# Kernel tuning notes

Measured on AMD Instinct MI355X. Metric: run time of the kernel, lower is better.

## Reference

```python
import math
import jax, jax.numpy as jnp
import numpy as np

HEADS = 16
MODEL = 1024
KEY = 64
VAL = 64
B, S = 4, 2048


def setup_inputs() -> dict:
    key = jax.random.key(0)
    ks = jax.random.split(key, 8)
    queries = jax.random.normal(ks[0], (B, S, MODEL), dtype=jnp.float32)
    keys_ = jax.random.normal(ks[1], (B, S, MODEL), dtype=jnp.float32)
    values = jax.random.normal(ks[2], (B, S, MODEL), dtype=jnp.float32)
    # causal boolean mask, true = attention allowed (every row has >=1 True)
    masks = jnp.broadcast_to(jnp.tril(jnp.ones((S, S), dtype=bool)), (B, S, S))
    lim_in = 1.0 / math.sqrt(MODEL)
    # stacked per-head projection weights, stored as [H, model, head_dim]
    Wq = jax.random.uniform(ks[3], (HEADS, MODEL, KEY), minval=-lim_in, maxval=lim_in, dtype=jnp.float32)
    Wk = jax.random.uniform(ks[4], (HEADS, MODEL, KEY), minval=-lim_in, maxval=lim_in, dtype=jnp.float32)
    Wv = jax.random.uniform(ks[5], (HEADS, MODEL, VAL), minval=-lim_in, maxval=lim_in, dtype=jnp.float32)
    lim_o = 1.0 / math.sqrt(HEADS * VAL)
    Wo = jax.random.uniform(ks[6], (HEADS * VAL, MODEL), minval=-lim_o, maxval=lim_o, dtype=jnp.float32)
    bo = jax.random.uniform(ks[7], (MODEL,), minval=-lim_o, maxval=lim_o, dtype=jnp.float32)
    return {"queries": queries, "keys": keys_, "values": values, "masks": masks,
            "Wq": Wq, "Wk": Wk, "Wv": Wv, "Wo": Wo, "bo": bo}


def reference(queries, keys, values, masks, Wq, Wk, Wv, Wo, bo):
    # per-head projections, batched over heads: [B,S,M] x [H,M,D] -> [B,H,S,D]
    q = jnp.einsum('bsm,hmd->bhsd', queries, Wq)
    k = jnp.einsum('bsm,hmd->bhsd', keys, Wk)
    v = jnp.einsum('bsm,hmd->bhsd', values, Wv)
    scale = 1.0 / math.sqrt(KEY)
    scores = jnp.einsum('bhqd,bhkd->bhqk', q, k) * scale  # [B,H,Q,K]
    scores = jnp.where(masks[:, None, :, :], scores, -jnp.inf)
    weights = jax.nn.softmax(scores, axis=-1)
    out = jnp.einsum('bhqk,bhkv->bhqv', weights, v)  # [B,H,Q,V]
    # concat heads along feature dim (head-major order matches torch concat)
    out = out.transpose(0, 2, 1, 3).reshape(B, S, HEADS * VAL)
    return out @ Wo + bo
```

## Files before the change

### kernel.cpp

```cpp
#include <hip/hip_runtime.h>


typedef __bf16 bf16;
typedef __attribute__((ext_vector_type(8))) __bf16 bf16x8;
typedef __attribute__((ext_vector_type(4))) __bf16 bf16x4;
typedef __attribute__((ext_vector_type(4))) float f32x4;
typedef unsigned int u32;

#define GLB_AS __attribute__((address_space(1)))
#define LDS_AS __attribute__((address_space(3)))

#define L2E 1.44269504088896340736f

static __device__ __forceinline__ void stage_swz(const bf16* __restrict__ g, long ldelem,
                                                 long row0, long col0,
                                                 bf16* lds, int rows, int tid)
{
    const int lane = tid & 63;
    const int wave = tid >> 6;
    const int nch = rows >> 3;
    for (int c = wave; c < nch; c += 4) {
        unsigned o  = ((unsigned)c << 10) + ((unsigned)lane << 4);
        unsigned r  = o >> 7;
        unsigned cb = o & 127u;
        unsigned cs = cb ^ ((r & 7u) << 4);
        const bf16* src = g + (row0 + (long)r) * ldelem + col0 + (long)(cs >> 1);
        char* dst = (char*)lds + ((unsigned)c << 10);
        __builtin_amdgcn_global_load_lds((GLB_AS u32*)src, (LDS_AS u32*)dst, 16, 0, 0);
    }
}

__global__ void cast3(const float4* __restrict__ a, const float4* __restrict__ b,
                      const float4* __restrict__ c,
                      bf16x4* __restrict__ xa, bf16x4* __restrict__ xb,
                      bf16x4* __restrict__ xc)
{
    const int n4 = (8192 * 1024) / 4;
    for (int i = blockIdx.x * blockDim.x + threadIdx.x; i < n4; i += gridDim.x * blockDim.x) {
        float4 v;
        v = a[i]; xa[i] = (bf16x4){(bf16)v.x, (bf16)v.y, (bf16)v.z, (bf16)v.w};
        v = b[i]; xb[i] = (bf16x4){(bf16)v.x, (bf16)v.y, (bf16)v.z, (bf16)v.w};
        v = c[i]; xc[i] = (bf16x4){(bf16)v.x, (bf16)v.y, (bf16)v.z, (bf16)v.w};
    }
}

__global__ void transw(const float* __restrict__ wq, const float* __restrict__ wk,
                       const float* __restrict__ wv, const float* __restrict__ wo,
                       bf16* __restrict__ wqT, bf16* __restrict__ wkT,
                       bf16* __restrict__ wvT, bf16* __restrict__ woT)
{
    __shared__ float t[64][65];
    const int tid = threadIdx.x, bx = blockIdx.x, by = blockIdx.y;
    const float* srcs[3] = {wq, wk, wv};
    bf16* dsts[3] = {wqT, wkT, wvT};
#pragma unroll
    for (int m = 0; m < 3; ++m) {
        const float sc = (m == 0) ? 0.125f : 1.0f;
        for (int i = tid; i < 4096; i += 256) {
            int r = i >> 6, c = i & 63;
            t[c][r] = srcs[m][by * 65536 + (bx * 64 + r) * 64 + c];
        }
        __syncthreads();
        for (int i = tid; i < 4096; i += 256) {
            int r = i >> 6, c = i & 63;
            dsts[m][(long)(by * 64 + r) * 1024 + bx * 64 + c] = (bf16)(t[r][c] * sc);
        }
        __syncthreads();
    }
    for (int i = tid; i < 4096; i += 256) {
        int r = i >> 6, c = i & 63;
        t[c][r] = wo[(long)(bx * 64 + r) * 1024 + by * 64 + c];
    }
    __syncthreads();
    for (int i = tid; i < 4096; i += 256) {
        int r = i >> 6, c = i & 63;
        woT[(long)(by * 64 + r) * 1024 + bx * 64 + c] = (bf16)t[r][c];
    }
}

template<int MODE>
static __device__ __forceinline__ void gemm_body(const bf16* __restrict__ A,
                                                 const bf16* __restrict__ Bt,
                                                 bf16* __restrict__ Cb,
                                                 float* __restrict__ Cf,
                                                 const float* __restrict__ bias,
                                                 long row0, long col0,
                                                 bf16* sA, bf16* sB)
{
    const int tid = threadIdx.x, lane = tid & 63, wave = tid >> 6;
    const int wr = wave >> 1, wc = wave & 1;

    f32x4 acc[4][4];
#pragma unroll
    for (int i = 0; i < 4; ++i)
#pragma unroll
        for (int j = 0; j < 4; ++j) acc[i][j] = (f32x4){0.f, 0.f, 0.f, 0.f};

    for (int kt = 0; kt < 16; ++kt) {
        __syncthreads();
        stage_swz(A,  1024, row0, (long)kt << 6, sA, 128, tid);
        stage_swz(Bt, 1024, col0, (long)kt << 6, sB, 128, tid);
        __syncthreads();
#pragma unroll
        for (int kk = 0; kk < 2; ++kk) {
            bf16x8 af[4], bfr[4];
            const unsigned kb = (unsigned)(kk << 6) + (unsigned)((lane >> 4) << 4);
#pragma unroll
            for (int i = 0; i < 4; ++i) {
                unsigned r = (unsigned)((wr << 6) + (i << 4) + (lane & 15));
                af[i] = *(const bf16x8*)((const char*)sA + (r << 7) + (kb ^ ((r & 7u) << 4)));
            }
#pragma unroll
            for (int j = 0; j < 4; ++j) {
                unsigned r = (unsigned)((wc << 6) + (j << 4) + (lane & 15));
                bfr[j] = *(const bf16x8*)((const char*)sB + (r << 7) + (kb ^ ((r & 7u) << 4)));
            }
#pragma unroll
            for (int i = 0; i < 4; ++i)
#pragma unroll
                for (int j = 0; j < 4; ++j)
                    acc[i][j] = __builtin_amdgcn_mfma_f32_16x16x32_bf16(af[i], bfr[j], acc[i][j], 0, 0, 0);
        }
    }

#pragma unroll
    for (int i = 0; i < 4; ++i) {
#pragma unroll
        for (int j = 0; j < 4; ++j) {
#pragma unroll
            for (int rr = 0; rr < 4; ++rr) {
                long row = row0 + (wr << 6) + (i << 4) + ((lane >> 4) << 2) + rr;
                long col = col0 + (wc << 6) + (j << 4) + (lane & 15);
                float v = acc[i][j][rr];
                if constexpr (MODE == 2) {
                    Cf[row * 1024 + col] = v + bias[col];
                } else if constexpr (MODE == 0) {
                    long idx = (((row >> 11) << 4) + (col >> 6)) * 131072 + (row & 2047) * 64 + (col & 63);
                    Cb[idx] = (bf16)v;
                } else {
                    long idx = ((((col >> 11) << 4) + (row >> 6)) * 64 + (row & 63)) * 2048 + (col & 2047);
                    Cb[idx] = (bf16)v;
                }
            }
        }
    }
}

__global__ __launch_bounds__(256, 3) void gemm_qkv(const bf16* __restrict__ Xq, const bf16* __restrict__ WqT, bf16* __restrict__ qp,
                                                   const bf16* __restrict__ Xk, const bf16* __restrict__ WkT, bf16* __restrict__ kp,
                                                   const bf16* __restrict__ WvT, const bf16* __restrict__ Xv, bf16* __restrict__ vTp)
{
    __shared__ alignas(16) bf16 sA[128 * 64];
    __shared__ alignas(16) bf16 sB[128 * 64];
    const int bx = blockIdx.x;
    if (blockIdx.y == 0)
        gemm_body<0>(Xq, WqT, qp, nullptr, nullptr, (long)(bx >> 3) << 7, (long)(bx & 7) << 7, sA, sB);
    else if (blockIdx.y == 1)
        gemm_body<0>(Xk, WkT, kp, nullptr, nullptr, (long)(bx >> 3) << 7, (long)(bx & 7) << 7, sA, sB);
    else
        gemm_body<3>(WvT, Xv, vTp, nullptr, nullptr, (long)(bx & 7) << 7, (long)(bx >> 3) << 7, sA, sB);
}

__global__ __launch_bounds__(256, 3) void gemm_out(const bf16* __restrict__ A, const bf16* __restrict__ Bt,
                                                   float* __restrict__ Cf, const float* __restrict__ bias)
{
    __shared__ alignas(16) bf16 sA[128 * 64];
    __shared__ alignas(16) bf16 sB[128 * 64];
    gemm_body<2>(A, Bt, nullptr, Cf, bias, (long)blockIdx.x << 7, (long)blockIdx.y << 7, sA, sB);
}

__global__ __launch_bounds__(256, 2) void attn(const bf16* __restrict__ q,
                                               const bf16* __restrict__ k,
                                               const bf16* __restrict__ vT,
                                               bf16* __restrict__ o)
{
    __shared__ alignas(16) bf16 sK[2][64 * 64];
    __shared__ alignas(16) bf16 sV[2][64 * 64];
    __shared__ alignas(16) bf16 sP[4][32 * 72];
    const int tid = threadIdx.x, lane = tid & 63, wave = tid >> 6;
    const int bid = blockIdx.x;
    const int hb = ((bid & 7) << 3) + ((bid >> 3) & 7);
    const int pair = bid >> 6;
    const int h = hb & 15, b = hb >> 4;
    const bf16* qh = q  + (long)hb * 131072;
    const bf16* kh = k  + (long)hb * 131072;
    const bf16* vh = vT + (long)hb * 131072;

    bf16x8 vone;
#pragma unroll
    for (int i = 0; i < 8; ++i) vone[i] = (bf16)1.0f;

    for (int half = 0; half < 2; ++half) {
        const int qt = half ? (15 - pair) : pair;
        const int qw = (qt << 7) + (wave << 5);

        bf16x8 aq[2][2];
#pragma unroll
        for (int mf = 0; mf < 2; ++mf)
#pragma unroll
            for (int kk = 0; kk < 2; ++kk)
                aq[mf][kk] = *(const bf16x8*)(qh + (long)(qw + (mf << 4) + (lane & 15)) * 64
                                                 + (kk << 5) + ((lane >> 4) << 3));

        f32x4 accO[2][4], accOl[2];
        float mrow[2][4];
#pragma unroll
        for (int mf = 0; mf < 2; ++mf) {
#pragma unroll
            for (int nf = 0; nf < 4; ++nf) accO[mf][nf] = (f32x4){0.f, 0.f, 0.f, 0.f};
            accOl[mf] = (f32x4){0.f, 0.f, 0.f, 0.f};
#pragma unroll
            for (int rr = 0; rr < 4; ++rr) mrow[mf][rr] = -1e30f;
        }

        const int nkv = (qt << 1) + 2;
        __syncthreads();
        stage_swz(kh, 64,   0, 0, sK[0], 64, tid);
        stage_swz(vh, 2048, 0, 0, sV[0], 64, tid);

        for (int kvt = 0; kvt < nkv; ++kvt) {
            const int cur = kvt & 1;
            const int kv0 = kvt << 6;
            __syncthreads();
            if (kvt + 1 < nkv) {
                stage_swz(kh, 64,   (long)(kv0 + 64), 0, sK[cur ^ 1], 64, tid);
                stage_swz(vh, 2048, 0, (long)(kv0 + 64), sV[cur ^ 1], 64, tid);
            }
            if (kv0 > qw + 31) continue;

            f32x4 s[2][4];
#pragma unroll
            for (int mf = 0; mf < 2; ++mf)
#pragma unroll
                for (int nf = 0; nf < 4; ++nf) s[mf][nf] = (f32x4){0.f, 0.f, 0.f, 0.f};
#pragma unroll
            for (int kk = 0; kk < 2; ++kk) {
                bf16x8 bk[4];
                const unsigned kb = (unsigned)(kk << 6) + (unsigned)((lane >> 4) << 4);
#pragma unroll
                for (int nf = 0; nf < 4; ++nf) {
                    unsigned r = (unsigned)((nf << 4) + (lane & 15));
                    bk[nf] = *(const bf16x8*)((const char*)sK[cur] + (r << 7) + (kb ^ ((r & 7u) << 4)));
                }
#pragma unroll
                for (int mf = 0; mf < 2; ++mf)
#pragma unroll
                    for (int nf = 0; nf < 4; ++nf)
                        s[mf][nf] = __builtin_amdgcn_mfma_f32_16x16x32_bf16(aq[mf][kk], bk[nf], s[mf][nf], 0, 0, 0);
            }

            if (kv0 + 63 > qw) {
#pragma unroll
                for (int mf = 0; mf < 2; ++mf)
#pragma unroll
                    for (int rr = 0; rr < 4; ++rr) {
                        const int ra = qw + (mf << 4) + ((lane >> 4) << 2) + rr;
#pragma unroll
                        for (int nf = 0; nf < 4; ++nf)
                            if ((kv0 + (nf << 4) + (lane & 15)) > ra) s[mf][nf][rr] = -1e30f;
                    }
            }

#pragma unroll
            for (int mf = 0; mf < 2; ++mf) {
#pragma unroll
                for (int rr = 0; rr < 4; ++rr) {
                    float mt = fmaxf(fmaxf(s[mf][0][rr], s[mf][1][rr]), fmaxf(s[mf][2][rr], s[mf][3][rr]));
                    mt = fmaxf(mt, __shfl_xor(mt, 1));
                    mt = fmaxf(mt, __shfl_xor(mt, 2));
                    mt = fmaxf(mt, __shfl_xor(mt, 4));
                    mt = fmaxf(mt, __shfl_xor(mt, 8));
                    if (mt > mrow[mf][rr]) {
                        const float cf = __builtin_exp2f((mrow[mf][rr] - mt) * L2E);
                        mrow[mf][rr] = mt;
                        accOl[mf][rr] *= cf;
#pragma unroll
                        for (int nf = 0; nf < 4; ++nf) accO[mf][nf][rr] *= cf;
                    }
                    const float m2 = mrow[mf][rr] * L2E;
#pragma unroll
                    for (int nf = 0; nf < 4; ++nf)
                        s[mf][nf][rr] = __builtin_exp2f(__builtin_fmaf(s[mf][nf][rr], L2E, -m2));
                }
            }

            bf16* pw = &sP[wave][0];
#pragma unroll
            for (int mf = 0; mf < 2; ++mf)
#pragma unroll
                for (int nf = 0; nf < 4; ++nf)
#pragma unroll
                    for (int rr = 0; rr < 4; ++rr)
                        pw[((mf << 4) + ((lane >> 4) << 2) + rr) * 72 + (nf << 4) + (lane & 15)] =
                            (bf16)s[mf][nf][rr];

#pragma unroll
            for (int kk = 0; kk < 2; ++kk) {
                bf16x8 pa[2], bv[4];
#pragma unroll
                for (int mf = 0; mf < 2; ++mf)
                    pa[mf] = *(const bf16x8*)(pw + ((mf << 4) + (lane & 15)) * 72
                                                 + (kk << 5) + ((lane >> 4) << 3));
                const unsigned kb = (unsigned)(kk << 6) + (unsigned)((lane >> 4) << 4);
#pragma unroll
                for (int nf = 0; nf < 4; ++nf) {
                    unsigned r = (unsigned)((nf << 4) + (lane & 15));
                    bv[nf] = *(const bf16x8*)((const char*)sV[cur] + (r << 7) + (kb ^ ((r & 7u) << 4)));
                }
#pragma unroll
                for (int mf = 0; mf < 2; ++mf) {
#pragma unroll
                    for (int nf = 0; nf < 4; ++nf)
                        accO[mf][nf] = __builtin_amdgcn_mfma_f32_16x16x32_bf16(pa[mf], bv[nf], accO[mf][nf], 0, 0, 0);
                    accOl[mf] = __builtin_amdgcn_mfma_f32_16x16x32_bf16(pa[mf], vone, accOl[mf], 0, 0, 0);
                }
            }
        }

#pragma unroll
        for (int mf = 0; mf < 2; ++mf)
#pragma unroll
            for (int rr = 0; rr < 4; ++rr) {
                const float inv = 1.f / accOl[mf][rr];
                const long ra = qw + (mf << 4) + ((lane >> 4) << 2) + rr;
#pragma unroll
                for (int nf = 0; nf < 4; ++nf)
                    o[((long)b * 2048 + ra) * 1024 + (h << 6) + (nf << 4) + (lane & 15)] =
                        (bf16)(accO[mf][nf][rr] * inv);
            }
    }
}

extern "C" void kernel_launch(void* const* d_in, const int* in_sizes, int n_in,
                              void* d_out, int out_size, void* d_ws, size_t ws_size,
                              hipStream_t stream)
{
    const float* queries = (const float*)d_in[0];
    const float* keys    = (const float*)d_in[1];
    const float* values  = (const float*)d_in[2];
    const float* Wq = (const float*)d_in[4];
    const float* Wk = (const float*)d_in[5];
    const float* Wv = (const float*)d_in[6];
    const float* Wo = (const float*)d_in[7];
    const float* bo = (const float*)d_in[8];
    float* out = (float*)d_out;

    bf16* Xq  = (bf16*)d_ws;
    bf16* Xk  = Xq  + 8388608;
    bf16* Xv  = Xk  + 8388608;
    bf16* WqT = Xv  + 8388608;
    bf16* WkT = WqT + 1048576;
    bf16* WvT = WkT + 1048576;
    bf16* WoT = WvT + 1048576;
    bf16* qp  = WoT + 1048576;
    bf16* kp  = qp  + 8388608;
    bf16* vTp = Xq;
    bf16* ao  = Xk;
    if (ws_size < (size_t)92274688) return;

    cast3<<<dim3(2048), dim3(256), 0, stream>>>((const float4*)queries, (const float4*)keys,
                                                (const float4*)values,
                                                (bf16x4*)Xq, (bf16x4*)Xk, (bf16x4*)Xv);
    transw<<<dim3(16, 16), dim3(256), 0, stream>>>(Wq, Wk, Wv, Wo, WqT, WkT, WvT, WoT);
    gemm_qkv<<<dim3(512, 3), dim3(256), 0, stream>>>(Xq, WqT, qp, Xk, WkT, kp, WvT, Xv, vTp);
    attn<<<dim3(512), dim3(256), 0, stream>>>(qp, kp, vTp, ao);
    gemm_out<<<dim3(64, 8), dim3(256), 0, stream>>>(ao, WoT, out, bo);
}
```

Baseline: 440.3 us.

## Transpose score MFMA so softmax rows reduce in-lane with lazy rescaling

Swaps the MFMA operands so each lane holds one query row's scores across registers. The row max then needs only two cross-lane shuffles instead of four per register row. The running max is updated only when it grows by more than a threshold, and the accumulator rescale is skipped for the whole wave unless some lane updated. P is written to LDS as packed 4-element vector stores. Together these cut shuffle, exp and LDS store instructions in the softmax, at the cost of slightly larger unnormalized exponent values that bf16/fp32 must absorb.

```diff
diff --git a/kernel.cpp b/kernel.cpp
--- a/kernel.cpp
+++ b/kernel.cpp
@@ -203,14 +203,13 @@
                                                  + (kk << 5) + ((lane >> 4) << 3));
 
         f32x4 accO[2][4], accOl[2];
-        float mrow[2][4];
+        float mrow[2];
 #pragma unroll
         for (int mf = 0; mf < 2; ++mf) {
 #pragma unroll
             for (int nf = 0; nf < 4; ++nf) accO[mf][nf] = (f32x4){0.f, 0.f, 0.f, 0.f};
             accOl[mf] = (f32x4){0.f, 0.f, 0.f, 0.f};
-#pragma unroll
-            for (int rr = 0; rr < 4; ++rr) mrow[mf][rr] = -1e30f;
+            mrow[mf] = -1e30f;
         }
 
         const int nkv = (qt << 1) + 2;
@@ -246,60 +245,75 @@
                 for (int mf = 0; mf < 2; ++mf)
 #pragma unroll
                     for (int nf = 0; nf < 4; ++nf)
-                        s[mf][nf] = __builtin_amdgcn_mfma_f32_16x16x32_bf16(aq[mf][kk], bk[nf], s[mf][nf], 0, 0, 0);
-            }
+                        s[mf][nf] = __builtin_amdgcn_mfma_f32_16x16x32_bf16(bk[nf], aq[mf][kk], s[mf][nf], 0, 0, 0);
+            }
+
+            const int g4 = (lane >> 4) << 2;
 
             if (kv0 + 63 > qw) {
 #pragma unroll
+                for (int mf = 0; mf < 2; ++mf) {
+                    const int qv = qw + (mf << 4) + (lane & 15);
+#pragma unroll
+                    for (int nf = 0; nf < 4; ++nf)
+#pragma unroll
+                        for (int reg = 0; reg < 4; ++reg)
+                            if (kv0 + (nf << 4) + g4 + reg > qv) s[mf][nf][reg] = -1e30f;
+                }
+            }
+
+            bool upAny = false;
+            float cfl[2];
+#pragma unroll
+            for (int mf = 0; mf < 2; ++mf) {
+                float m0 = fmaxf(fmaxf(s[mf][0][0], s[mf][0][1]), fmaxf(s[mf][0][2], s[mf][0][3]));
+                float m1 = fmaxf(fmaxf(s[mf][1][0], s[mf][1][1]), fmaxf(s[mf][1][2], s[mf][1][3]));
+                float m2_ = fmaxf(fmaxf(s[mf][2][0], s[mf][2][1]), fmaxf(s[mf][2][2], s[mf][2][3]));
+                float m3 = fmaxf(fmaxf(s[mf][3][0], s[mf][3][1]), fmaxf(s[mf][3][2], s[mf][3][3]));
+                float mt = fmaxf(fmaxf(m0, m1), fmaxf(m2_, m3));
+                mt = fmaxf(mt, __shfl_xor(mt, 16));
+                mt = fmaxf(mt, __shfl_xor(mt, 32));
+                const bool up = mt > mrow[mf] + 8.0f;
+                cfl[mf] = up ? __builtin_exp2f((mrow[mf] - mt) * L2E) : 1.0f;
+                if (up) mrow[mf] = mt;
+                upAny = upAny || up;
+                const float mm = mrow[mf] * L2E;
+#pragma unroll
+                for (int nf = 0; nf < 4; ++nf)
+#pragma unroll
+                    for (int reg = 0; reg < 4; ++reg)
+                        s[mf][nf][reg] = __builtin_exp2f(__builtin_fmaf(s[mf][nf][reg], L2E, -mm));
+            }
+            if (__any(upAny)) {
+#pragma unroll
                 for (int mf = 0; mf < 2; ++mf)
 #pragma unroll
-                    for (int rr = 0; rr < 4; ++rr) {
-                        const int ra = qw + (mf << 4) + ((lane >> 4) << 2) + rr;
-#pragma unroll
-                        for (int nf = 0; nf < 4; ++nf)
-                            if ((kv0 + (nf << 4) + (lane & 15)) > ra) s[mf][nf][rr] = -1e30f;
+                    for (int reg = 0; reg < 4; ++reg) {
+                        const float c = __shfl(cfl[mf], g4 + reg);
+                        accOl[mf][reg] *= c;
+#pragma unroll
+                        for (int nf = 0; nf < 4; ++nf) accO[mf][nf][reg] *= c;
                     }
             }
 
+            bf16* pw = &sP[wave][0];
 #pragma unroll
             for (int mf = 0; mf < 2; ++mf) {
-#pragma unroll
-                for (int rr = 0; rr < 4; ++rr) {
-                    float mt = fmaxf(fmaxf(s[mf][0][rr], s[mf][1][rr]), fmaxf(s[mf][2][rr], s[mf][3][rr]));
-                    mt = fmaxf(mt, __shfl_xor(mt, 1));
-                    mt = fmaxf(mt, __shfl_xor(mt, 2));
-                    mt = fmaxf(mt, __shfl_xor(mt, 4));
-                    mt = fmaxf(mt, __shfl_xor(mt, 8));
-                    if (mt > mrow[mf][rr]) {
-                        const float cf = __builtin_exp2f((mrow[mf][rr] - mt) * L2E);
-                        mrow[mf][rr] = mt;
-                        accOl[mf][rr] *= cf;
-#pragma unroll
-                        for (int nf = 0; nf < 4; ++nf) accO[mf][nf][rr] *= cf;
-                    }
-                    const float m2 = mrow[mf][rr] * L2E;
-#pragma unroll
-                    for (int nf = 0; nf < 4; ++nf)
-                        s[mf][nf][rr] = __builtin_exp2f(__builtin_fmaf(s[mf][nf][rr], L2E, -m2));
-                }
-            }
-
-            bf16* pw = &sP[wave][0];
-#pragma unroll
-            for (int mf = 0; mf < 2; ++mf)
-#pragma unroll
-                for (int nf = 0; nf < 4; ++nf)
-#pragma unroll
-                    for (int rr = 0; rr < 4; ++rr)
-                        pw[((mf << 4) + ((lane >> 4) << 2) + rr) * 72 + (nf << 4) + (lane & 15)] =
-                            (bf16)s[mf][nf][rr];
+                bf16* pp = pw + ((mf << 4) + (lane & 15)) * 72 + g4;
+#pragma unroll
+                for (int nf = 0; nf < 4; ++nf) {
+                    bf16x4 pv = {(bf16)s[mf][nf][0], (bf16)s[mf][nf][1],
+                                 (bf16)s[mf][nf][2], (bf16)s[mf][nf][3]};
+                    *(bf16x4*)(pp + (nf << 4)) = pv;
+                }
+            }
 
 #pragma unroll
             for (int kk = 0; kk < 2; ++kk) {
                 bf16x8 pa[2], bv[4];
 #pragma unroll
                 for (int mf = 0; mf < 2; ++mf)
-                    pa[mf] = *(const bf16x8*)(pw + ((mf << 4) + (lane & 15)) * 72
+                    pa[mf] = *(const bf16x8*)(pw + (((mf << 4) + (lane & 15)) * 72)
                                                  + (kk << 5) + ((lane >> 4) << 3));
                 const unsigned kb = (unsigned)(kk << 6) + (unsigned)((lane >> 4) << 4);
 #pragma unroll
```

Result: faster. 406.9 us (-7.6%).
